# Performance work log

Measured on AMD Instinct MI355X. Metric: run time of the kernel, lower is better.

Reference implementation:

```python
import jax, jax.numpy as jnp
import numpy as np


def setup_inputs() -> dict:
    key = jax.random.key(0)
    ks = jax.random.split(key, 5)
    B, T, C, HS = 8, 2048, 1024, 64
    return {
        "x_q": jax.random.normal(ks[0], (B, T, C), dtype=jnp.float32),
        "x_kv": jax.random.normal(ks[1], (B, T, C), dtype=jnp.float32),
        "Wq": jax.random.normal(ks[2], (C, HS), dtype=jnp.float32) * (C ** -0.5),
        "Wk": jax.random.normal(ks[3], (C, HS), dtype=jnp.float32) * (C ** -0.5),
        "Wv": jax.random.normal(ks[4], (C, HS), dtype=jnp.float32) * (C ** -0.5),
    }


def reference(x_q, x_kv, Wq, Wk, Wv):
    # x_q, x_kv: [B, T, C]; W*: [C, HS]
    B, T, C = x_q.shape
    q = jnp.einsum("btc,ch->bth", x_q, Wq)   # [B, T, HS]
    k = jnp.einsum("btc,ch->bth", x_kv, Wk)  # [B, T, HS]
    v = jnp.einsum("btc,ch->bth", x_kv, Wv)  # [B, T, HS]
    # NOTE: original scales by d_model**-0.5 (C), not head_size**-0.5
    wei = jnp.einsum("bqh,bkh->bqk", q, k) * (C ** -0.5)  # [B, T, T]
    causal = jnp.tril(jnp.ones((T, T), dtype=bool))
    wei = jnp.where(causal, wei, -jnp.inf)
    wei = jax.nn.softmax(wei, axis=-1)
    out = jnp.einsum("bqk,bkh->bqh", wei, v)  # [B, T, HS]
    return out
```

## Files before the change

kernel.cpp:

```cpp
#include <hip/hip_runtime.h>

typedef __bf16 bf16_t;
typedef __bf16 bf16x8 __attribute__((ext_vector_type(8)));
typedef float f32x4 __attribute__((ext_vector_type(4)));
typedef unsigned short u16x4 __attribute__((ext_vector_type(4)));

#define B_ 8
#define T_ 2048
#define C_ 1024
#define HS_ 64
#define VSTRIDE 2080

#define MFMA __builtin_amdgcn_mfma_f32_16x16x32_bf16

__device__ __forceinline__ float fast_exp2(float x) {
#if __has_builtin(__builtin_amdgcn_exp2f)
  return __builtin_amdgcn_exp2f(x);
#else
  return exp2f(x);
#endif
}

__device__ __forceinline__ void async_ld16(const void* gsrc, void* lds_dst) {
  __builtin_amdgcn_global_load_lds(
      (const __attribute__((address_space(1))) void*)gsrc,
      (__attribute__((address_space(3))) void*)lds_dst, 16, 0, 0);
}

__global__ __launch_bounds__(256) void repack_w(
    const float* __restrict__ Wq, const float* __restrict__ Wk,
    const float* __restrict__ Wv, bf16_t* __restrict__ pq,
    bf16_t* __restrict__ pk, bf16_t* __restrict__ pv) {
  const float* W = (blockIdx.y == 0) ? Wq : ((blockIdx.y == 1) ? Wk : Wv);
  bf16_t* P = (blockIdx.y == 0) ? pq : ((blockIdx.y == 1) ? pk : pv);
  int t = blockIdx.x * 256 + threadIdx.x;
  int lane = t & 63, nt = (t >> 6) & 3, kc = t >> 8;
  int quad = lane >> 4, ln = lane & 15;
  bf16x8 v;
#pragma unroll
  for (int j = 0; j < 8; ++j)
    v[j] = (bf16_t)W[(kc * 32 + quad * 8 + j) * HS_ + nt * 16 + ln];
  *(bf16x8*)(P + (size_t)t * 8) = v;
}

template <bool KV>
__global__ __launch_bounds__(256) void proj_mfma(
    const float* __restrict__ x, const bf16_t* __restrict__ pA,
    const bf16_t* __restrict__ pB, bf16_t* __restrict__ outA,
    bf16_t* __restrict__ vT) {
  __shared__ float Xb[2][64][128];
  __shared__ bf16_t Bb[2][KV ? 2 : 1][16][512];

  const int w = threadIdx.x >> 6, lane = threadIdx.x & 63;
  const int quad = lane >> 4, ln = lane & 15;
  const int m0blk = blockIdx.x * 64;
  const int m0 = m0blk + w * 16;
  const int l32 = lane & 31, lhalf = lane >> 5;

  f32x4 acc0[4], acc1[4];
#pragma unroll
  for (int nt = 0; nt < 4; ++nt) {
    acc0[nt] = (f32x4){0.f, 0.f, 0.f, 0.f};
    acc1[nt] = (f32x4){0.f, 0.f, 0.f, 0.f};
  }

  auto STAGE = [&](int c, int buf) {
#pragma unroll
    for (int i = 0; i < 8; ++i) {
      const int row = w * 16 + 2 * i + lhalf;
      const int sg = l32 ^ (row & 7);
      async_ld16(x + (size_t)(m0blk + row) * C_ + c * 128 + sg * 4,
                 &Xb[buf][w * 16 + 2 * i][0]);
    }
#pragma unroll
    for (int j = 0; j < 4; ++j) {
      const int p = w * 4 + j;
      async_ld16(pA + (size_t)(c * 16 + p) * 512 + lane * 8,
                 &Bb[buf][0][p][0]);
    }
    if constexpr (KV) {
#pragma unroll
      for (int j = 0; j < 4; ++j) {
        const int p = w * 4 + j;
        async_ld16(pB + (size_t)(c * 16 + p) * 512 + lane * 8,
                   &Bb[buf][1][p][0]);
      }
    }
  };

  auto COMPUTE = [&](int c, int buf) {
    const int swz = (ln & 7) << 4;
    const char* rp = (const char*)&Xb[buf][w * 16 + ln][0];
#pragma unroll
    for (int kc2 = 0; kc2 < 4; ++kc2) {
      f32x4 xlo = *(const f32x4*)(rp + ((kc2 * 128 + quad * 32) ^ swz));
      f32x4 xhi = *(const f32x4*)(rp + ((kc2 * 128 + quad * 32 + 16) ^ swz));
      bf16x8 a;
#pragma unroll
      for (int j = 0; j < 4; ++j) {
        a[j] = (bf16_t)xlo[j];
        a[4 + j] = (bf16_t)xhi[j];
      }
#pragma unroll
      for (int nt = 0; nt < 4; ++nt) {
        bf16x8 b0 = *(const bf16x8*)&Bb[buf][0][kc2 * 4 + nt][lane * 8];
        acc0[nt] = MFMA(a, b0, acc0[nt], 0, 0, 0);
      }
      if constexpr (KV) {
#pragma unroll
        for (int nt = 0; nt < 4; ++nt) {
          bf16x8 b1 = *(const bf16x8*)&Bb[buf][1][kc2 * 4 + nt][lane * 8];
          acc1[nt] = MFMA(a, b1, acc1[nt], 0, 0, 0);
        }
      }
    }
  };

#define WAIT_CHUNK()                                        \
  do {                                                      \
    if constexpr (KV)                                       \
      asm volatile("s_waitcnt vmcnt(16)" ::: "memory");     \
    else                                                    \
      asm volatile("s_waitcnt vmcnt(12)" ::: "memory");     \
  } while (0)

  STAGE(0, 0);
  STAGE(1, 1);
  WAIT_CHUNK();
  __builtin_amdgcn_s_barrier();
  __builtin_amdgcn_sched_barrier(0);

#pragma unroll
  for (int c = 0; c < 8; ++c) {
    COMPUTE(c, c & 1);
    if (c == 7) break;
    asm volatile("s_waitcnt lgkmcnt(0)" ::: "memory");
    __builtin_amdgcn_s_barrier();
    __builtin_amdgcn_sched_barrier(0);
    if (c < 6) {
      STAGE(c + 2, c & 1);
      WAIT_CHUNK();
    } else {
      asm volatile("s_waitcnt vmcnt(0)" ::: "memory");
    }
    __builtin_amdgcn_s_barrier();
    __builtin_amdgcn_sched_barrier(0);
  }
#undef WAIT_CHUNK

  if constexpr (!KV) {
#pragma unroll
    for (int nt = 0; nt < 4; ++nt)
#pragma unroll
      for (int r = 0; r < 4; ++r)
        outA[(size_t)(m0 + quad * 4 + r) * HS_ + nt * 16 + ln] =
            (bf16_t)acc0[nt][r];
  } else {
#pragma unroll
    for (int nt = 0; nt < 4; ++nt)
#pragma unroll
      for (int r = 0; r < 4; ++r)
        outA[(size_t)(m0 + quad * 4 + r) * HS_ + nt * 16 + ln] =
            (bf16_t)acc0[nt][r];
    const int bb = m0 >> 11, t0 = m0 & (T_ - 1);
#pragma unroll
    for (int nt = 0; nt < 4; ++nt) {
      u16x4 pk4;
#pragma unroll
      for (int r = 0; r < 4; ++r) {
        bf16_t h = (bf16_t)acc1[nt][r];
        pk4[r] = *(unsigned short*)&h;
      }
      *(u16x4*)((unsigned short*)vT +
                ((size_t)(bb * HS_ + nt * 16 + ln)) * VSTRIDE + t0 + quad * 4) =
          pk4;
    }
  }
}

__global__ __launch_bounds__(512) void attn_mfma(
    const bf16_t* __restrict__ q, const bf16_t* __restrict__ k,
    const bf16_t* __restrict__ vT, float* __restrict__ out) {
  __shared__ bf16_t p_lds[8][16][80];
  __shared__ float o_buf[8][16][66];
  __shared__ float l_buf[8][16][17];

  const int b = blockIdx.x >> 7;
  const int gq = blockIdx.x & 127;
  const int w = threadIdx.x >> 6, lane = threadIdx.x & 63;
  const int quad = lane >> 4, ln = lane & 15;
  const int qr0 = gq * 16;
  const size_t bt = (size_t)b * T_;
  const int td = gq >> 2;

  bf16x8 aq[2];
#pragma unroll
  for (int hc = 0; hc < 2; ++hc)
    aq[hc] = *(const bf16x8*)(q + (bt + qr0 + ln) * HS_ + hc * 32 + quad * 8);

  f32x4 o_acc[4];
  float l_part[4] = {0.f, 0.f, 0.f, 0.f};
#pragma unroll
  for (int nt = 0; nt < 4; ++nt) o_acc[nt] = (f32x4){0.f, 0.f, 0.f, 0.f};
  const float scl = 0.03125f * 1.44269504088896340736f;

  for (int t = w; t <= td; t += 8) {
    const int kr0 = t * 64;

    f32x4 s[4];
#pragma unroll
    for (int nt = 0; nt < 4; ++nt) s[nt] = (f32x4){0.f, 0.f, 0.f, 0.f};
#pragma unroll
    for (int hc = 0; hc < 2; ++hc)
#pragma unroll
      for (int nt = 0; nt < 4; ++nt) {
        bf16x8 bk = *(const bf16x8*)(k + (bt + kr0 + nt * 16 + ln) * HS_ +
                                     hc * 32 + quad * 8);
        s[nt] = MFMA(aq[hc], bk, s[nt], 0, 0, 0);
      }

    const bool diag = (t == td);
#pragma unroll
    for (int nt = 0; nt < 4; ++nt)
#pragma unroll
      for (int r = 0; r < 4; ++r) {
        float e = fast_exp2(s[nt][r] * scl);
        if (diag && (kr0 + nt * 16 + ln > qr0 + quad * 4 + r)) e = 0.f;
        l_part[r] += e;
        p_lds[w][quad * 4 + r][nt * 16 + ln] = (bf16_t)e;
      }

#pragma unroll
    for (int kc = 0; kc < 2; ++kc) {
      bf16x8 ap = *(const bf16x8*)&p_lds[w][ln][kc * 32 + quad * 8];
#pragma unroll
      for (int nt = 0; nt < 4; ++nt) {
        bf16x8 bv = *(const bf16x8*)(vT +
                                     ((size_t)(b * HS_ + nt * 16 + ln)) * VSTRIDE +
                                     kr0 + kc * 32 + quad * 8);
        o_acc[nt] = MFMA(ap, bv, o_acc[nt], 0, 0, 0);
      }
    }
  }

#pragma unroll
  for (int nt = 0; nt < 4; ++nt)
#pragma unroll
    for (int r = 0; r < 4; ++r)
      o_buf[w][quad * 4 + r][nt * 16 + ln] = o_acc[nt][r];
#pragma unroll
  for (int r = 0; r < 4; ++r) l_buf[w][quad * 4 + r][ln] = l_part[r];
  __syncthreads();

#pragma unroll
  for (int rr = 0; rr < 2; ++rr) {
    const int row = w + rr * 8;
    float o = 0.f, lsum = 0.f;
#pragma unroll
    for (int ww = 0; ww < 8; ++ww) {
      o += o_buf[ww][row][lane];
      lsum += l_buf[ww][row][lane & 15];
    }
#pragma unroll
    for (int off = 1; off < 16; off <<= 1) lsum += __shfl_xor(lsum, off);
    out[(bt + qr0 + row) * HS_ + lane] = o / lsum;
  }
}

extern "C" void kernel_launch(void* const* d_in, const int* in_sizes, int n_in,
                              void* d_out, int out_size, void* d_ws,
                              size_t ws_size, hipStream_t stream) {
  (void)in_sizes; (void)n_in; (void)out_size; (void)ws_size;
  const float* xq = (const float*)d_in[0];
  const float* xkv = (const float*)d_in[1];
  const float* Wq = (const float*)d_in[2];
  const float* Wk = (const float*)d_in[3];
  const float* Wv = (const float*)d_in[4];
  float* out = (float*)d_out;

  char* ws = (char*)d_ws;
  bf16_t* q = (bf16_t*)ws;
  bf16_t* kk = (bf16_t*)(ws + (2u << 20));
  bf16_t* vT = (bf16_t*)(ws + (4u << 20));
  bf16_t* pq = (bf16_t*)(ws + (6656u << 10));
  bf16_t* pk = (bf16_t*)(ws + (6784u << 10));
  bf16_t* pv = (bf16_t*)(ws + (6912u << 10));

  repack_w<<<dim3(32, 3), 256, 0, stream>>>(Wq, Wk, Wv, pq, pk, pv);
  proj_mfma<false><<<dim3(256), 256, 0, stream>>>(xq, pq, nullptr, q, nullptr);
  proj_mfma<true><<<dim3(256), 256, 0, stream>>>(xkv, pk, pv, kk, vT);
  attn_mfma<<<dim3(1024), 512, 0, stream>>>(q, kk, vT, out);
}
```

Measured before the change: 206.6 us.

## Merge projection launches, reorder attention blocks, prefetch K/V tiles into registers

Fuses the Q and KV projection kernels into one launch that selects its role from blockIdx.y, so the two projections run concurrently and one launch is saved. The attention grid is reordered to schedule the heaviest causal query blocks first and to interleave batches, and a min-blocks launch bound is added. Within the attention loop, the next K tile is prefetched into registers and the V tile is loaded before the QK MFMAs to hide global-load latency. The costs are higher register pressure under the tighter launch bound and a runtime branch in the projection kernel where there was a template.

```diff
diff --git a/kernel.cpp b/kernel.cpp
--- a/kernel.cpp
+++ b/kernel.cpp
@@ -43,13 +43,19 @@
   *(bf16x8*)(P + (size_t)t * 8) = v;
 }
 
-template <bool KV>
 __global__ __launch_bounds__(256) void proj_mfma(
-    const float* __restrict__ x, const bf16_t* __restrict__ pA,
-    const bf16_t* __restrict__ pB, bf16_t* __restrict__ outA,
-    bf16_t* __restrict__ vT) {
+    const float* __restrict__ xq, const float* __restrict__ xkv,
+    const bf16_t* __restrict__ pq, const bf16_t* __restrict__ pk,
+    const bf16_t* __restrict__ pv, bf16_t* __restrict__ q,
+    bf16_t* __restrict__ k, bf16_t* __restrict__ vT) {
   __shared__ float Xb[2][64][128];
-  __shared__ bf16_t Bb[2][KV ? 2 : 1][16][512];
+  __shared__ bf16_t Bb[2][2][16][512];
+
+  const bool is_kv = (blockIdx.y != 0);
+  const float* x = is_kv ? xkv : xq;
+  const bf16_t* pA = is_kv ? pk : pq;
+  const bf16_t* pB = pv;
+  bf16_t* outA = is_kv ? k : q;
 
   const int w = threadIdx.x >> 6, lane = threadIdx.x & 63;
   const int quad = lane >> 4, ln = lane & 15;
@@ -78,7 +84,7 @@
       async_ld16(pA + (size_t)(c * 16 + p) * 512 + lane * 8,
                  &Bb[buf][0][p][0]);
     }
-    if constexpr (KV) {
+    if (is_kv) {
 #pragma unroll
       for (int j = 0; j < 4; ++j) {
         const int p = w * 4 + j;
@@ -88,7 +94,7 @@
     }
   };
 
-  auto COMPUTE = [&](int c, int buf) {
+  auto COMPUTE = [&](int buf) {
     const int swz = (ln & 7) << 4;
     const char* rp = (const char*)&Xb[buf][w * 16 + ln][0];
 #pragma unroll
@@ -106,7 +112,7 @@
         bf16x8 b0 = *(const bf16x8*)&Bb[buf][0][kc2 * 4 + nt][lane * 8];
         acc0[nt] = MFMA(a, b0, acc0[nt], 0, 0, 0);
       }
-      if constexpr (KV) {
+      if (is_kv) {
 #pragma unroll
         for (int nt = 0; nt < 4; ++nt) {
           bf16x8 b1 = *(const bf16x8*)&Bb[buf][1][kc2 * 4 + nt][lane * 8];
@@ -118,7 +124,7 @@
 
 #define WAIT_CHUNK()                                        \
   do {                                                      \
-    if constexpr (KV)                                       \
+    if (is_kv)                                              \
       asm volatile("s_waitcnt vmcnt(16)" ::: "memory");     \
     else                                                    \
       asm volatile("s_waitcnt vmcnt(12)" ::: "memory");     \
@@ -132,7 +138,7 @@
 
 #pragma unroll
   for (int c = 0; c < 8; ++c) {
-    COMPUTE(c, c & 1);
+    COMPUTE(c & 1);
     if (c == 7) break;
     asm volatile("s_waitcnt lgkmcnt(0)" ::: "memory");
     __builtin_amdgcn_s_barrier();
@@ -148,20 +154,13 @@
   }
 #undef WAIT_CHUNK
 
-  if constexpr (!KV) {
-#pragma unroll
-    for (int nt = 0; nt < 4; ++nt)
-#pragma unroll
-      for (int r = 0; r < 4; ++r)
-        outA[(size_t)(m0 + quad * 4 + r) * HS_ + nt * 16 + ln] =
-            (bf16_t)acc0[nt][r];
-  } else {
-#pragma unroll
-    for (int nt = 0; nt < 4; ++nt)
-#pragma unroll
-      for (int r = 0; r < 4; ++r)
-        outA[(size_t)(m0 + quad * 4 + r) * HS_ + nt * 16 + ln] =
-            (bf16_t)acc0[nt][r];
+#pragma unroll
+  for (int nt = 0; nt < 4; ++nt)
+#pragma unroll
+    for (int r = 0; r < 4; ++r)
+      outA[(size_t)(m0 + quad * 4 + r) * HS_ + nt * 16 + ln] =
+          (bf16_t)acc0[nt][r];
+  if (is_kv) {
     const int bb = m0 >> 11, t0 = m0 & (T_ - 1);
 #pragma unroll
     for (int nt = 0; nt < 4; ++nt) {
@@ -178,15 +177,15 @@
   }
 }
 
-__global__ __launch_bounds__(512) void attn_mfma(
+__global__ __launch_bounds__(512, 4) void attn_mfma(
     const bf16_t* __restrict__ q, const bf16_t* __restrict__ k,
     const bf16_t* __restrict__ vT, float* __restrict__ out) {
   __shared__ bf16_t p_lds[8][16][80];
   __shared__ float o_buf[8][16][66];
   __shared__ float l_buf[8][16][17];
 
-  const int b = blockIdx.x >> 7;
-  const int gq = blockIdx.x & 127;
+  const int b = blockIdx.x & 7;
+  const int gq = 127 - (blockIdx.x >> 3);
   const int w = threadIdx.x >> 6, lane = threadIdx.x & 63;
   const int quad = lane >> 4, ln = lane & 15;
   const int qr0 = gq * 16;
@@ -204,20 +203,46 @@
   for (int nt = 0; nt < 4; ++nt) o_acc[nt] = (f32x4){0.f, 0.f, 0.f, 0.f};
   const float scl = 0.03125f * 1.44269504088896340736f;
 
-  for (int t = w; t <= td; t += 8) {
+  bf16x8 bk[8], bv[8];
+  int t = w;
+  if (t <= td) {
+#pragma unroll
+    for (int hc = 0; hc < 2; ++hc)
+#pragma unroll
+      for (int nt = 0; nt < 4; ++nt)
+        bk[hc * 4 + nt] = *(const bf16x8*)(k + (bt + t * 64 + nt * 16 + ln) * HS_ +
+                                           hc * 32 + quad * 8);
+  }
+
+  for (; t <= td; t += 8) {
     const int kr0 = t * 64;
 
+#pragma unroll
+    for (int kc = 0; kc < 2; ++kc)
+#pragma unroll
+      for (int nt = 0; nt < 4; ++nt)
+        bv[kc * 4 + nt] = *(const bf16x8*)(vT +
+                                           ((size_t)(b * HS_ + nt * 16 + ln)) * VSTRIDE +
+                                           kr0 + kc * 32 + quad * 8);
+
     f32x4 s[4];
 #pragma unroll
     for (int nt = 0; nt < 4; ++nt) s[nt] = (f32x4){0.f, 0.f, 0.f, 0.f};
 #pragma unroll
     for (int hc = 0; hc < 2; ++hc)
 #pragma unroll
-      for (int nt = 0; nt < 4; ++nt) {
-        bf16x8 bk = *(const bf16x8*)(k + (bt + kr0 + nt * 16 + ln) * HS_ +
-                                     hc * 32 + quad * 8);
-        s[nt] = MFMA(aq[hc], bk, s[nt], 0, 0, 0);
-      }
+      for (int nt = 0; nt < 4; ++nt)
+        s[nt] = MFMA(aq[hc], bk[hc * 4 + nt], s[nt], 0, 0, 0);
+
+    if (t + 8 <= td) {
+#pragma unroll
+      for (int hc = 0; hc < 2; ++hc)
+#pragma unroll
+        for (int nt = 0; nt < 4; ++nt)
+          bk[hc * 4 + nt] = *(const bf16x8*)(k +
+                                             (bt + (t + 8) * 64 + nt * 16 + ln) * HS_ +
+                                             hc * 32 + quad * 8);
+    }
 
     const bool diag = (t == td);
 #pragma unroll
@@ -234,12 +259,8 @@
     for (int kc = 0; kc < 2; ++kc) {
       bf16x8 ap = *(const bf16x8*)&p_lds[w][ln][kc * 32 + quad * 8];
 #pragma unroll
-      for (int nt = 0; nt < 4; ++nt) {
-        bf16x8 bv = *(const bf16x8*)(vT +
-                                     ((size_t)(b * HS_ + nt * 16 + ln)) * VSTRIDE +
-                                     kr0 + kc * 32 + quad * 8);
-        o_acc[nt] = MFMA(ap, bv, o_acc[nt], 0, 0, 0);
-      }
+      for (int nt = 0; nt < 4; ++nt)
+        o_acc[nt] = MFMA(ap, bv[kc * 4 + nt], o_acc[nt], 0, 0, 0);
     }
   }
 
@@ -287,7 +308,6 @@
   bf16_t* pv = (bf16_t*)(ws + (6912u << 10));
 
   repack_w<<<dim3(32, 3), 256, 0, stream>>>(Wq, Wk, Wv, pq, pk, pv);
-  proj_mfma<false><<<dim3(256), 256, 0, stream>>>(xq, pq, nullptr, q, nullptr);
-  proj_mfma<true><<<dim3(256), 256, 0, stream>>>(xkv, pk, pv, kk, vT);
+  proj_mfma<<<dim3(256, 2), 256, 0, stream>>>(xq, xkv, pq, pk, pv, q, kk, vT);
   attn_mfma<<<dim3(1024), 512, 0, stream>>>(q, kk, vT, out);
 }
```

New measurement: 198.2 us. 4.1% less time.
